# Kernel tuning notes

Measured on AMD Instinct MI355X. Metric: run time of the kernel, lower is better.

The kernel has to match this reference:

```python
import jax, jax.numpy as jnp
import numpy as np

N_NODES = 65536
N_GRAPHS = 1024
NODES_PER_G = 64
N_EDGES = 1048576
IN_FEATS = 512
HIDDEN = 1024
H4 = 256
EMB = 512
EPS = 1e-5
SLOPE = 0.01


def setup_inputs() -> dict:
    key = jax.random.key(0)
    ks = jax.random.split(key, 10)
    # within-graph random edges: edge e belongs to graph e // (E/B)
    epg = N_EDGES // N_GRAPHS
    eg = np.arange(N_EDGES) // epg
    rng = np.random.default_rng(0)
    src = rng.integers(0, NODES_PER_G, N_EDGES) + eg * NODES_PER_G
    dst = rng.integers(0, NODES_PER_G, N_EDGES) + eg * NODES_PER_G
    node_gid = np.arange(N_NODES) // NODES_PER_G
    return {
        "node_feats": jax.random.normal(ks[0], (N_NODES, IN_FEATS), jnp.float32),
        "edge_weights": jax.random.uniform(ks[1], (N_EDGES,), jnp.float32),
        "W1": jax.random.normal(ks[2], (IN_FEATS, HIDDEN), jnp.float32) * 0.05,
        "W2": jax.random.normal(ks[3], (HIDDEN, H4), jnp.float32) * 0.05,
        "W_emb": jax.random.normal(ks[4], (IN_FEATS + HIDDEN + H4, EMB), jnp.float32) * 0.02,
        "gn1_alpha": jnp.ones((HIDDEN,), jnp.float32),
        "gn1_gamma": jnp.ones((HIDDEN,), jnp.float32),
        "gn1_beta": jnp.zeros((HIDDEN,), jnp.float32),
        "gn2_alpha": jnp.ones((H4,), jnp.float32),
        "gn2_gamma": jnp.ones((H4,), jnp.float32),
        "gn2_beta": jnp.zeros((H4,), jnp.float32),
        "edge_src": jnp.asarray(src, jnp.int32),
        "edge_dst": jnp.asarray(dst, jnp.int32),
        "node_gid": jnp.asarray(node_gid, jnp.int32),
    }


def _seg_sum(x, ids, num):
    return jax.ops.segment_sum(x, ids, num_segments=num)


def _graph_conv(x, W, src, dst, ew):
    # DGL GraphConv, norm='both', bias=False, with edge_weight (u_mul_e)
    ones = jnp.ones((src.shape[0],), x.dtype)
    deg_out = jnp.clip(_seg_sum(ones, src, N_NODES), 1.0)
    deg_in = jnp.clip(_seg_sum(ones, dst, N_NODES), 1.0)
    h = (x * jax.lax.rsqrt(deg_out)[:, None]) @ W
    msg = h[src] * ew[:, None]
    agg = _seg_sum(msg, dst, N_NODES)
    return agg * jax.lax.rsqrt(deg_in)[:, None]


def _graph_norm(x, gid, counts, alpha, gamma, beta):
    # GraphNorm (Cai et al.): learnable mean-scale alpha, per-graph stats
    mean = _seg_sum(x, gid, N_GRAPHS) / counts[:, None]
    sub = x - alpha * mean[gid]
    var = _seg_sum(sub * sub, gid, N_GRAPHS) / counts[:, None]
    return gamma * sub * jax.lax.rsqrt(var[gid] + EPS) + beta


def _mean_nodes(x, gid, counts):
    return _seg_sum(x, gid, N_GRAPHS) / counts[:, None]


def _leaky(x):
    return jnp.where(x >= 0, x, SLOPE * x)


def reference(node_feats, edge_weights, W1, W2, W_emb,
              gn1_alpha, gn1_gamma, gn1_beta,
              gn2_alpha, gn2_gamma, gn2_beta,
              edge_src, edge_dst, node_gid):
    counts = jnp.clip(_seg_sum(jnp.ones((N_NODES,), node_feats.dtype), node_gid, N_GRAPHS), 1.0)
    r0 = _mean_nodes(node_feats, node_gid, counts)                 # [B, in]
    h1 = _graph_conv(node_feats, W1, edge_src, edge_dst, edge_weights)
    h1 = _leaky(_graph_norm(h1, node_gid, counts, gn1_alpha, gn1_gamma, gn1_beta))
    r1 = _mean_nodes(h1, node_gid, counts)                          # [B, hidden]
    h2 = _graph_conv(h1, W2, edge_src, edge_dst, edge_weights)
    h2 = _leaky(_graph_norm(h2, node_gid, counts, gn2_alpha, gn2_gamma, gn2_beta))
    r2 = _mean_nodes(h2, node_gid, counts)                          # [B, hidden/4]
    emb = jnp.concatenate([r0, r1, r2], axis=1) @ W_emb             # [B, EMB]
    # InstanceNorm1d on [B, E] input: per-row normalization, no affine
    mu = jnp.mean(emb, axis=1, keepdims=True)
    var = jnp.mean((emb - mu) ** 2, axis=1, keepdims=True)
    emb = (emb - mu) * jax.lax.rsqrt(var + EPS)
    return _leaky(emb)
```

## Files before the change

### kernel.cpp

```cpp
#include <hip/hip_runtime.h>
#include <hip/hip_bf16.h>
#include <stdint.h>

#define N_NODES   65536
#define N_GRAPHS  1024
#define N_EDGES   1048576
#define IN_FEATS  512
#define HIDDEN    1024
#define H4        256
#define EMB_DIM   512
#define RDIM      1792
#define EPS_F     1e-5f
#define SLOPE_F   0.01f

typedef __bf16 bf16;
typedef __bf16 bf16x8 __attribute__((ext_vector_type(8)));
typedef float  floatx4 __attribute__((ext_vector_type(4)));

#define GLDS16(gp, lp) __builtin_amdgcn_global_load_lds( \
    (const __attribute__((address_space(1))) void*)(gp), \
    (__attribute__((address_space(3))) void*)(lp), 16, 0, 0)

__global__ __launch_bounds__(256) void k_graph_build(
    const int* __restrict__ src, const int* __restrict__ dst,
    const float* __restrict__ ew,
    bf16* __restrict__ adjb, float* __restrict__ scl_o)
{
    __shared__ float sAdj[4096];
    __shared__ float sDegO[64], sDegI[64];
    int g = blockIdx.x, tid = threadIdx.x;
    for (int i = tid; i < 4096; i += 256) sAdj[i] = 0.f;
    if (tid < 64) { sDegO[tid] = 0.f; sDegI[tid] = 0.f; }
    __syncthreads();
    int e0 = g * 1024;
    #pragma unroll
    for (int i = 0; i < 4; ++i) {
        int e = e0 + i * 256 + tid;
        int s = src[e] & 63, d = dst[e] & 63;
        atomicAdd(&sAdj[(d << 6) | s], ew[e]);
        atomicAdd(&sDegO[s], 1.f);
        atomicAdd(&sDegI[d], 1.f);
    }
    __syncthreads();
    if (tid < 64) scl_o[g * 64 + tid] = rsqrtf(fmaxf(sDegO[tid], 1.f));
    bf16* ag = adjb + ((size_t)g << 12);
    for (int i = tid; i < 4096; i += 256) {
        float si = rsqrtf(fmaxf(sDegI[i >> 6], 1.f));
        ag[i] = (bf16)(sAdj[i] * si);
    }
}

__global__ __launch_bounds__(256) void k_transpose(
    const float* __restrict__ W, bf16* __restrict__ WT, int K, int logN)
{
    int idx = blockIdx.x * 256 + threadIdx.x;
    if (idx >= (K << logN)) return;
    int n = idx & ((1 << logN) - 1);
    int k = idx >> logN;
    WT[(size_t)n * K + k] = (bf16)W[idx];
}

__global__ __launch_bounds__(256) void k_prep_agg1(
    const float* __restrict__ x, const float* __restrict__ so,
    const bf16* __restrict__ adjb,
    bf16* __restrict__ axs1, bf16* __restrict__ Rb)
{
    __shared__ __align__(16) bf16 sOut[64 * 264];
    __shared__ float sSo[64];
    int g = blockIdx.x >> 1, half = blockIdx.x & 1;
    int tid = threadIdx.x, lane = tid & 63, wave = tid >> 6, q = lane >> 4;
    if (tid < 64) sSo[tid] = so[g * 64 + tid];
    const float* xg = x + (size_t)g * 64 * IN_FEATS + half * 256;
    const bf16* ag = adjb + ((size_t)g << 12);

    bf16x8 af[4][2];
    #pragma unroll
    for (int mt = 0; mt < 4; ++mt)
        #pragma unroll
        for (int kk = 0; kk < 2; ++kk)
            af[mt][kk] = *(const bf16x8*)&ag[(mt * 16 + (lane & 15)) * 64 + kk * 32 + q * 8];
    __syncthreads();
    float sov[2][8];
    #pragma unroll
    for (int kk = 0; kk < 2; ++kk)
        #pragma unroll
        for (int j = 0; j < 8; ++j) sov[kk][j] = sSo[kk * 32 + q * 8 + j];

    #pragma unroll
    for (int nt = 0; nt < 4; ++nt) {
        int cl = wave * 64 + nt * 16 + (lane & 15);
        floatx4 acc[4] = {};
        float r0 = 0.f;
        #pragma unroll
        for (int kk = 0; kk < 2; ++kk) {
            bf16x8 bfrag;
            #pragma unroll
            for (int j = 0; j < 8; ++j) {
                float v = xg[(size_t)(kk * 32 + q * 8 + j) * IN_FEATS + cl];
                r0 += v;
                bfrag[j] = (bf16)(v * sov[kk][j]);
            }
            #pragma unroll
            for (int mt = 0; mt < 4; ++mt)
                acc[mt] = __builtin_amdgcn_mfma_f32_16x16x32_bf16(af[mt][kk], bfrag, acc[mt], 0, 0, 0);
        }
        r0 += __shfl_xor(r0, 16);
        r0 += __shfl_xor(r0, 32);
        if (lane < 16) Rb[(size_t)g * RDIM + half * 256 + cl] = (bf16)(r0 * (1.f / 64.f));
        #pragma unroll
        for (int mt = 0; mt < 4; ++mt)
            #pragma unroll
            for (int i = 0; i < 4; ++i)
                sOut[(mt * 16 + q * 4 + i) * 264 + cl] = (bf16)acc[mt][i];
    }
    __syncthreads();
    #pragma unroll
    for (int it = 0; it < 8; ++it) {
        int idx = it * 256 + tid;
        int d = idx >> 5, c8 = idx & 31;
        *(bf16x8*)&axs1[(size_t)(g * 64 + d) * IN_FEATS + half * 256 + c8 * 8] =
            *(const bf16x8*)&sOut[d * 264 + c8 * 8];
    }
}

__device__ __forceinline__ void gemm_mainloop(
    const bf16* __restrict__ A, const bf16* __restrict__ BT, int K,
    int row0, int col0, int lane, int wave, int wm, int wn, int q,
    bf16* sA, bf16* sB, floatx4 (&acc)[4][4])
{
    for (int k0 = 0; k0 < K; k0 += 64) {
        #pragma unroll
        for (int i = 0; i < 4; ++i) {
            int u = (wave * 4 + i) * 64 + lane;
            int r = u >> 3, p = u & 7;
            int c = p ^ (r & 7);
            GLDS16(A  + (size_t)(row0 + r) * K + (k0 + c * 8), &sA[(wave * 4 + i) * 512]);
            GLDS16(BT + (size_t)(col0 + r) * K + (k0 + c * 8), &sB[(wave * 4 + i) * 512]);
        }
        asm volatile("s_waitcnt vmcnt(0)" ::: "memory");
        __syncthreads();
        #pragma unroll
        for (int kk = 0; kk < 64; kk += 32) {
            bf16x8 afr[4], bfr[4];
            #pragma unroll
            for (int mt = 0; mt < 4; ++mt) {
                int r = wm * 64 + mt * 16 + (lane & 15);
                int c = (kk >> 3) + q;
                afr[mt] = *(const bf16x8*)&sA[(r * 8 + (c ^ (r & 7))) * 8];
            }
            #pragma unroll
            for (int nt = 0; nt < 4; ++nt) {
                int r = wn * 64 + nt * 16 + (lane & 15);
                int c = (kk >> 3) + q;
                bfr[nt] = *(const bf16x8*)&sB[(r * 8 + (c ^ (r & 7))) * 8];
            }
            #pragma unroll
            for (int mt = 0; mt < 4; ++mt)
                #pragma unroll
                for (int nt = 0; nt < 4; ++nt)
                    acc[mt][nt] = __builtin_amdgcn_mfma_f32_16x16x32_bf16(
                        afr[mt], bfr[nt], acc[mt][nt], 0, 0, 0);
        }
        __syncthreads();
    }
}

__device__ __forceinline__ void swizzle_block(int cb, int& bx, int& by)
{
    int b = blockIdx.y * gridDim.x + blockIdx.x;
    int xcd = b & 7, t = b >> 3;
    bx = t % cb;
    by = (t / cb) * 8 + xcd;
}

__global__ __launch_bounds__(256) void k_gemm1_f(
    const bf16* __restrict__ A, const bf16* __restrict__ BT,
    const float* __restrict__ alpha, const float* __restrict__ gamma,
    const float* __restrict__ beta,
    const float* __restrict__ so,
    bf16* __restrict__ xs2, bf16* __restrict__ Rb)
{
    __shared__ __align__(16) bf16 sm[128 * 136];
    __shared__ float sSo[128];
    bf16* sA = sm;
    bf16* sB = sm + 8192;
    const int tid = threadIdx.x;
    const int lane = tid & 63, wave = tid >> 6, q = lane >> 4;
    const int wm = wave & 1, wn = wave >> 1;
    int bx, by; swizzle_block(gridDim.x, bx, by);
    const int row0 = by * 128, col0 = bx * 128;

    if (tid < 128) sSo[tid] = so[row0 + tid];

    floatx4 acc[4][4] = {};
    gemm_mainloop(A, BT, IN_FEATS, row0, col0, lane, wave, wm, wn, q, sA, sB, acc);

    const int gw = by * 2 + wm;
    bf16* sOut = sm;
    #pragma unroll
    for (int nt = 0; nt < 4; ++nt) {
        int cl = wn * 64 + nt * 16 + (lane & 15);
        int colg = col0 + cl;
        float lsum = 0.f;
        #pragma unroll
        for (int mt = 0; mt < 4; ++mt)
            #pragma unroll
            for (int i = 0; i < 4; ++i) lsum += acc[mt][nt][i];
        lsum += __shfl_xor(lsum, 16);
        lsum += __shfl_xor(lsum, 32);
        float am = alpha[colg] * (lsum * (1.f / 64.f));
        float gm = gamma[colg], bt = beta[colg];
        float sub[4][4], qv = 0.f;
        #pragma unroll
        for (int mt = 0; mt < 4; ++mt)
            #pragma unroll
            for (int i = 0; i < 4; ++i) {
                float d = acc[mt][nt][i] - am;
                sub[mt][i] = d; qv += d * d;
            }
        qv += __shfl_xor(qv, 16);
        qv += __shfl_xor(qv, 32);
        float rs = rsqrtf(qv * (1.f / 64.f) + EPS_F);
        float rsum = 0.f;
        #pragma unroll
        for (int mt = 0; mt < 4; ++mt)
            #pragma unroll
            for (int i = 0; i < 4; ++i) {
                float o = gm * sub[mt][i] * rs + bt;
                o = (o >= 0.f) ? o : SLOPE_F * o;
                rsum += o;
                int r = wm * 64 + mt * 16 + q * 4 + i;
                sOut[r * 136 + cl] = (bf16)(o * sSo[r]);
            }
        rsum += __shfl_xor(rsum, 16);
        rsum += __shfl_xor(rsum, 32);
        if (lane < 16)
            Rb[(size_t)gw * RDIM + 512 + colg] = (bf16)(rsum * (1.f / 64.f));
    }
    __syncthreads();
    #pragma unroll
    for (int it = 0; it < 8; ++it) {
        int idx = it * 256 + tid;
        int r = idx >> 4, c8 = idx & 15;
        *(bf16x8*)&xs2[(size_t)(row0 + r) * HIDDEN + col0 + c8 * 8] =
            *(const bf16x8*)&sOut[r * 136 + c8 * 8];
    }
}

__global__ __launch_bounds__(256) void k_gemm2_f(
    const bf16* __restrict__ A, const bf16* __restrict__ BT,
    const bf16* __restrict__ adjb,
    const float* __restrict__ alpha, const float* __restrict__ gamma,
    const float* __restrict__ beta,
    bf16* __restrict__ Rb)
{
    __shared__ __align__(16) bf16 sm[128 * 136];
    bf16* sA = sm;
    bf16* sB = sm + 8192;
    const int tid = threadIdx.x;
    const int lane = tid & 63, wave = tid >> 6, q = lane >> 4;
    const int wm = wave & 1, wn = wave >> 1;
    int bx, by; swizzle_block(gridDim.x, bx, by);
    const int row0 = by * 128, col0 = bx * 128;

    floatx4 acc[4][4] = {};
    gemm_mainloop(A, BT, HIDDEN, row0, col0, lane, wave, wm, wn, q, sA, sB, acc);

    bf16* sT = sm;
    #pragma unroll
    for (int nt = 0; nt < 4; ++nt) {
        int cl = wn * 64 + nt * 16 + (lane & 15);
        #pragma unroll
        for (int mt = 0; mt < 4; ++mt)
            #pragma unroll
            for (int i = 0; i < 4; ++i)
                sT[cl * 136 + wm * 64 + mt * 16 + q * 4 + i] = (bf16)acc[mt][nt][i];
    }
    asm volatile("s_waitcnt lgkmcnt(0)" ::: "memory");

    const int gw = by * 2 + wm;
    const bf16* ag = adjb + ((size_t)gw << 12);
    floatx4 a2[4][4] = {};
    #pragma unroll
    for (int kk = 0; kk < 2; ++kk) {
        bf16x8 afr[4], bfr[4];
        #pragma unroll
        for (int mt = 0; mt < 4; ++mt)
            afr[mt] = *(const bf16x8*)&ag[(mt * 16 + (lane & 15)) * 64 + kk * 32 + q * 8];
        #pragma unroll
        for (int nt = 0; nt < 4; ++nt)
            bfr[nt] = *(const bf16x8*)&sT[(wn * 64 + nt * 16 + (lane & 15)) * 136 + wm * 64 + kk * 32 + q * 8];
        #pragma unroll
        for (int mt = 0; mt < 4; ++mt)
            #pragma unroll
            for (int nt = 0; nt < 4; ++nt)
                a2[mt][nt] = __builtin_amdgcn_mfma_f32_16x16x32_bf16(afr[mt], bfr[nt], a2[mt][nt], 0, 0, 0);
    }

    #pragma unroll
    for (int nt = 0; nt < 4; ++nt) {
        int colg = col0 + wn * 64 + nt * 16 + (lane & 15);
        float lsum = 0.f;
        #pragma unroll
        for (int mt = 0; mt < 4; ++mt)
            #pragma unroll
            for (int i = 0; i < 4; ++i) lsum += a2[mt][nt][i];
        lsum += __shfl_xor(lsum, 16);
        lsum += __shfl_xor(lsum, 32);
        float am = alpha[colg] * (lsum * (1.f / 64.f));
        float gm = gamma[colg], bt = beta[colg];
        float sub[4][4], qv = 0.f;
        #pragma unroll
        for (int mt = 0; mt < 4; ++mt)
            #pragma unroll
            for (int i = 0; i < 4; ++i) {
                float d = a2[mt][nt][i] - am;
                sub[mt][i] = d; qv += d * d;
            }
        qv += __shfl_xor(qv, 16);
        qv += __shfl_xor(qv, 32);
        float rs = rsqrtf(qv * (1.f / 64.f) + EPS_F);
        float rsum = 0.f;
        #pragma unroll
        for (int mt = 0; mt < 4; ++mt)
            #pragma unroll
            for (int i = 0; i < 4; ++i) {
                float o = gm * sub[mt][i] * rs + bt;
                rsum += (o >= 0.f) ? o : SLOPE_F * o;
            }
        rsum += __shfl_xor(rsum, 16);
        rsum += __shfl_xor(rsum, 32);
        if (lane < 16)
            Rb[(size_t)gw * RDIM + 1536 + colg] = (bf16)(rsum * (1.f / 64.f));
    }
}

__global__ __launch_bounds__(256) void k_gemm_ro(
    const bf16* __restrict__ A, const bf16* __restrict__ BT,
    float* __restrict__ Cout)
{
    __shared__ __align__(16) bf16 sm[16384];
    bf16* sA = sm;
    bf16* sB = sm + 8192;
    const int tid = threadIdx.x;
    const int lane = tid & 63, wave = tid >> 6, q = lane >> 4;
    const int wm = wave & 1, wn = wave >> 1;
    int bx, by; swizzle_block(gridDim.x, bx, by);
    const int row0 = by * 128, col0 = bx * 128;

    floatx4 acc[4][4] = {};
    gemm_mainloop(A, BT, RDIM, row0, col0, lane, wave, wm, wn, q, sA, sB, acc);

    #pragma unroll
    for (int mt = 0; mt < 4; ++mt)
        #pragma unroll
        for (int nt = 0; nt < 4; ++nt) {
            int col = col0 + wn * 64 + nt * 16 + (lane & 15);
            #pragma unroll
            for (int i = 0; i < 4; ++i) {
                int row = row0 + wm * 64 + mt * 16 + q * 4 + i;
                Cout[(size_t)row * EMB_DIM + col] = acc[mt][nt][i];
            }
        }
}

__global__ __launch_bounds__(256) void k_instnorm(
    const float* __restrict__ emb, float* __restrict__ out)
{
    int row = blockIdx.x, tid = threadIdx.x;
    int lane = tid & 63, wave = tid >> 6;
    __shared__ float sS[4], sQ[4];
    float v0 = emb[(size_t)row * EMB_DIM + tid];
    float v1 = emb[(size_t)row * EMB_DIM + 256 + tid];
    float s = v0 + v1, q = v0 * v0 + v1 * v1;
    #pragma unroll
    for (int off = 32; off; off >>= 1) {
        s += __shfl_down(s, off);
        q += __shfl_down(q, off);
    }
    if (lane == 0) { sS[wave] = s; sQ[wave] = q; }
    __syncthreads();
    float S = sS[0] + sS[1] + sS[2] + sS[3];
    float Q = sQ[0] + sQ[1] + sQ[2] + sQ[3];
    float mu = S * (1.f / 512.f);
    float var = Q * (1.f / 512.f) - mu * mu;
    float rs = rsqrtf(var + EPS_F);
    float o0 = (v0 - mu) * rs; o0 = (o0 >= 0.f) ? o0 : SLOPE_F * o0;
    float o1 = (v1 - mu) * rs; o1 = (o1 >= 0.f) ? o1 : SLOPE_F * o1;
    out[(size_t)row * EMB_DIM + tid]       = o0;
    out[(size_t)row * EMB_DIM + 256 + tid] = o1;
}

extern "C" void kernel_launch(void* const* d_in, const int* in_sizes, int n_in,
                              void* d_out, int out_size, void* d_ws, size_t ws_size,
                              hipStream_t stream) {
    const float* x    = (const float*)d_in[0];
    const float* ew   = (const float*)d_in[1];
    const float* W1   = (const float*)d_in[2];
    const float* W2   = (const float*)d_in[3];
    const float* Wemb = (const float*)d_in[4];
    const float* a1   = (const float*)d_in[5];
    const float* g1   = (const float*)d_in[6];
    const float* b1   = (const float*)d_in[7];
    const float* a2   = (const float*)d_in[8];
    const float* g2   = (const float*)d_in[9];
    const float* b2   = (const float*)d_in[10];
    const int* esrc   = (const int*)d_in[11];
    const int* edst   = (const int*)d_in[12];
    float* out = (float*)d_out;

    char* ws = (char*)d_ws;
    const size_t MB = 1024ull * 1024ull;
    bf16*  adjb   = (bf16*)(ws);
    float* scl_o  = (float*)(ws + 8 * MB);
    bf16*  Rb     = (bf16*)(ws + 9 * MB);
    bf16*  W1T    = (bf16*)(ws + 13 * MB);
    bf16*  W2T    = (bf16*)(ws + 14 * MB);
    bf16*  WembT  = (bf16*)(ws + 15 * MB);
    float* emb    = (float*)(ws + 17 * MB);
    bf16*  axs1   = (bf16*)(ws + 20 * MB);
    bf16*  xs2    = (bf16*)(ws + 84 * MB);

    k_graph_build<<<N_GRAPHS, 256, 0, stream>>>(esrc, edst, ew, adjb, scl_o);
    k_transpose<<<2048, 256, 0, stream>>>(W1, W1T, 512, 10);
    k_transpose<<<1024, 256, 0, stream>>>(W2, W2T, 1024, 8);
    k_transpose<<<3584, 256, 0, stream>>>(Wemb, WembT, 1792, 9);

    k_prep_agg1<<<N_GRAPHS * 2, 256, 0, stream>>>(x, scl_o, adjb, axs1, Rb);

    k_gemm1_f<<<dim3(HIDDEN / 128, N_NODES / 128), 256, 0, stream>>>(
        axs1, W1T, a1, g1, b1, scl_o, xs2, Rb);
    k_gemm2_f<<<dim3(H4 / 128, N_NODES / 128), 256, 0, stream>>>(
        xs2, W2T, adjb, a2, g2, b2, Rb);
    k_gemm_ro<<<dim3(EMB_DIM / 128, N_GRAPHS / 128), 256, 0, stream>>>(
        Rb, WembT, emb);
    k_instnorm<<<N_GRAPHS, 256, 0, stream>>>(emb, out);

    (void)in_sizes; (void)n_in; (void)out_size; (void)ws_size;
}
```

Measured before the change: 490.7 us.

## Fuse layer-1 and layer-2 GEMMs into a per-graph kernel keeping hidden activations on-chip

Replaces the separate GEMM1 (with GraphNorm epilogue writing xs2 to global memory) and GEMM2 kernels with a single per-graph kernel. Each block loads its graph's 64x512 aggregated inputs into LDS, computes hidden features in 128-column chunks, applies GraphNorm, LeakyReLU and readout, then immediately accumulates the chunk into the layer-2 product. The layer-2 aggregation and norm run in the same block. This removes the 128MB xs2 round trip and one launch. In exchange, B fragments of W1T and W2T are read directly from global or L2 without LDS staging, and each block is serialised over 8 chunks with only 1024 blocks, which may lower occupancy and MFMA efficiency.

```diff
diff --git a/kernel.cpp b/kernel.cpp
--- a/kernel.cpp
+++ b/kernel.cpp
@@ -21,6 +21,8 @@
     (const __attribute__((address_space(1))) void*)(gp), \
     (__attribute__((address_space(3))) void*)(lp), 16, 0, 0)
 
+#define MFMA16(a, b, c) __builtin_amdgcn_mfma_f32_16x16x32_bf16((a), (b), (c), 0, 0, 0)
+
 __global__ __launch_bounds__(256) void k_graph_build(
     const int* __restrict__ src, const int* __restrict__ dst,
     const float* __restrict__ ew,
@@ -102,7 +104,7 @@
             }
             #pragma unroll
             for (int mt = 0; mt < 4; ++mt)
-                acc[mt] = __builtin_amdgcn_mfma_f32_16x16x32_bf16(af[mt][kk], bfrag, acc[mt], 0, 0, 0);
+                acc[mt] = MFMA16(af[mt][kk], bfrag, acc[mt]);
         }
         r0 += __shfl_xor(r0, 16);
         r0 += __shfl_xor(r0, 32);
@@ -120,6 +122,197 @@
         int d = idx >> 5, c8 = idx & 31;
         *(bf16x8*)&axs1[(size_t)(g * 64 + d) * IN_FEATS + half * 256 + c8 * 8] =
             *(const bf16x8*)&sOut[d * 264 + c8 * 8];
+    }
+}
+
+__global__ __launch_bounds__(256) void k_fused12(
+    const bf16* __restrict__ axs1, const bf16* __restrict__ W1T,
+    const bf16* __restrict__ W2T,  const bf16* __restrict__ adjb,
+    const float* __restrict__ so,
+    const float* __restrict__ a1v, const float* __restrict__ g1v,
+    const float* __restrict__ b1v,
+    const float* __restrict__ a2v, const float* __restrict__ g2v,
+    const float* __restrict__ b2v,
+    bf16* __restrict__ Rb)
+{
+    __shared__ __align__(16) bf16 sm[40960];
+    bf16* sA = sm;
+    bf16* sX = sm + 32768;
+
+    const int g = blockIdx.x, tid = threadIdx.x;
+    const int lane = tid & 63, wave = tid >> 6, q = lane >> 4, l15 = lane & 15;
+
+    const bf16* Ag = axs1 + (((size_t)g << 6) * IN_FEATS);
+    #pragma unroll
+    for (int i = 0; i < 16; ++i) {
+        int u = i * 256 + tid;
+        int r = u >> 6, cp = u & 63;
+        int c = cp ^ (r & 63);
+        GLDS16(Ag + ((size_t)r << 9) + (c << 3), &sA[(i * 256 + wave * 64) * 8]);
+    }
+    float sov[16];
+    #pragma unroll
+    for (int mt = 0; mt < 4; ++mt)
+        #pragma unroll
+        for (int i = 0; i < 4; ++i)
+            sov[mt * 4 + i] = so[g * 64 + mt * 16 + q * 4 + i];
+
+    floatx4 h2[4][4] = {};
+
+    asm volatile("s_waitcnt vmcnt(0)" ::: "memory");
+    __syncthreads();
+
+    for (int c = 0; c < 8; ++c) {
+        floatx4 acc[4][2] = {};
+        #pragma unroll 4
+        for (int ks = 0; ks < 16; ++ks) {
+            bf16x8 bfr[2];
+            #pragma unroll
+            for (int nt = 0; nt < 2; ++nt) {
+                int n = c * 128 + wave * 32 + nt * 16 + l15;
+                bfr[nt] = *(const bf16x8*)&W1T[((size_t)n << 9) + ks * 32 + q * 8];
+            }
+            bf16x8 afr[4];
+            #pragma unroll
+            for (int mt = 0; mt < 4; ++mt) {
+                int r = mt * 16 + l15;
+                int cu = (ks * 4 + q) ^ (r & 63);
+                afr[mt] = *(const bf16x8*)&sA[(r * 64 + cu) * 8];
+            }
+            #pragma unroll
+            for (int mt = 0; mt < 4; ++mt)
+                #pragma unroll
+                for (int nt = 0; nt < 2; ++nt)
+                    acc[mt][nt] = MFMA16(afr[mt], bfr[nt], acc[mt][nt]);
+        }
+        #pragma unroll
+        for (int nt = 0; nt < 2; ++nt) {
+            int cl = wave * 32 + nt * 16 + l15;
+            int colg = c * 128 + cl;
+            float lsum = 0.f;
+            #pragma unroll
+            for (int mt = 0; mt < 4; ++mt)
+                #pragma unroll
+                for (int i = 0; i < 4; ++i) lsum += acc[mt][nt][i];
+            lsum += __shfl_xor(lsum, 16);
+            lsum += __shfl_xor(lsum, 32);
+            float am = a1v[colg] * (lsum * (1.f / 64.f));
+            float gm = g1v[colg], bt = b1v[colg];
+            float sub[4][4], qv = 0.f;
+            #pragma unroll
+            for (int mt = 0; mt < 4; ++mt)
+                #pragma unroll
+                for (int i = 0; i < 4; ++i) {
+                    float d = acc[mt][nt][i] - am;
+                    sub[mt][i] = d; qv += d * d;
+                }
+            qv += __shfl_xor(qv, 16);
+            qv += __shfl_xor(qv, 32);
+            float rs = rsqrtf(qv * (1.f / 64.f) + EPS_F);
+            float rsum = 0.f;
+            int cu = cl >> 3, ce = cl & 7;
+            #pragma unroll
+            for (int mt = 0; mt < 4; ++mt)
+                #pragma unroll
+                for (int i = 0; i < 4; ++i) {
+                    float o = gm * sub[mt][i] * rs + bt;
+                    o = (o >= 0.f) ? o : SLOPE_F * o;
+                    rsum += o;
+                    int r = mt * 16 + q * 4 + i;
+                    sX[(r * 16 + (cu ^ (r & 15))) * 8 + ce] = (bf16)(o * sov[mt * 4 + i]);
+                }
+            rsum += __shfl_xor(rsum, 16);
+            rsum += __shfl_xor(rsum, 32);
+            if (lane < 16)
+                Rb[(size_t)g * RDIM + 512 + colg] = (bf16)(rsum * (1.f / 64.f));
+        }
+        __syncthreads();
+        #pragma unroll
+        for (int kk = 0; kk < 4; ++kk) {
+            bf16x8 afr[4], bfr[4];
+            #pragma unroll
+            for (int mt = 0; mt < 4; ++mt) {
+                int r = mt * 16 + l15;
+                int cu = (kk * 4 + q) ^ (r & 15);
+                afr[mt] = *(const bf16x8*)&sX[(r * 16 + cu) * 8];
+            }
+            #pragma unroll
+            for (int nt = 0; nt < 4; ++nt) {
+                int n = wave * 64 + nt * 16 + l15;
+                bfr[nt] = *(const bf16x8*)&W2T[((size_t)n << 10) + c * 128 + kk * 32 + q * 8];
+            }
+            #pragma unroll
+            for (int mt = 0; mt < 4; ++mt)
+                #pragma unroll
+                for (int nt = 0; nt < 4; ++nt)
+                    h2[mt][nt] = MFMA16(afr[mt], bfr[nt], h2[mt][nt]);
+        }
+        __syncthreads();
+    }
+
+    bf16* sT = sA + wave * (64 * 68);
+    #pragma unroll
+    for (int nt = 0; nt < 4; ++nt) {
+        int cl = nt * 16 + l15;
+        #pragma unroll
+        for (int mt = 0; mt < 4; ++mt)
+            #pragma unroll
+            for (int i = 0; i < 4; ++i)
+                sT[cl * 68 + mt * 16 + q * 4 + i] = (bf16)h2[mt][nt][i];
+    }
+    asm volatile("s_waitcnt lgkmcnt(0)" ::: "memory");
+    const bf16* ag = adjb + ((size_t)g << 12);
+    floatx4 fin[4][4] = {};
+    #pragma unroll
+    for (int kk = 0; kk < 2; ++kk) {
+        bf16x8 afr[4], bfr[4];
+        #pragma unroll
+        for (int mt = 0; mt < 4; ++mt)
+            afr[mt] = *(const bf16x8*)&ag[(mt * 16 + l15) * 64 + kk * 32 + q * 8];
+        #pragma unroll
+        for (int nt = 0; nt < 4; ++nt)
+            bfr[nt] = *(const bf16x8*)&sT[(nt * 16 + l15) * 68 + kk * 32 + q * 8];
+        #pragma unroll
+        for (int mt = 0; mt < 4; ++mt)
+            #pragma unroll
+            for (int nt = 0; nt < 4; ++nt)
+                fin[mt][nt] = MFMA16(afr[mt], bfr[nt], fin[mt][nt]);
+    }
+    #pragma unroll
+    for (int nt = 0; nt < 4; ++nt) {
+        int colg = wave * 64 + nt * 16 + l15;
+        float lsum = 0.f;
+        #pragma unroll
+        for (int mt = 0; mt < 4; ++mt)
+            #pragma unroll
+            for (int i = 0; i < 4; ++i) lsum += fin[mt][nt][i];
+        lsum += __shfl_xor(lsum, 16);
+        lsum += __shfl_xor(lsum, 32);
+        float am = a2v[colg] * (lsum * (1.f / 64.f));
+        float gm = g2v[colg], bt = b2v[colg];
+        float sub[4][4], qv = 0.f;
+        #pragma unroll
+        for (int mt = 0; mt < 4; ++mt)
+            #pragma unroll
+            for (int i = 0; i < 4; ++i) {
+                float d = fin[mt][nt][i] - am;
+                sub[mt][i] = d; qv += d * d;
+            }
+        qv += __shfl_xor(qv, 16);
+        qv += __shfl_xor(qv, 32);
+        float rs = rsqrtf(qv * (1.f / 64.f) + EPS_F);
+        float rsum = 0.f;
+        #pragma unroll
+        for (int mt = 0; mt < 4; ++mt)
+            #pragma unroll
+            for (int i = 0; i < 4; ++i) {
+                float o = gm * sub[mt][i] * rs + bt;
+                rsum += (o >= 0.f) ? o : SLOPE_F * o;
+            }
+        rsum += __shfl_xor(rsum, 16);
+        rsum += __shfl_xor(rsum, 32);
+        if (lane < 16)
+            Rb[(size_t)g * RDIM + 1536 + colg] = (bf16)(rsum * (1.f / 64.f));
     }
 }
 
@@ -158,180 +351,9 @@
             for (int mt = 0; mt < 4; ++mt)
                 #pragma unroll
                 for (int nt = 0; nt < 4; ++nt)
-                    acc[mt][nt] = __builtin_amdgcn_mfma_f32_16x16x32_bf16(
-                        afr[mt], bfr[nt], acc[mt][nt], 0, 0, 0);
+                    acc[mt][nt] = MFMA16(afr[mt], bfr[nt], acc[mt][nt]);
         }
         __syncthreads();
-    }
-}
-
-__device__ __forceinline__ void swizzle_block(int cb, int& bx, int& by)
-{
-    int b = blockIdx.y * gridDim.x + blockIdx.x;
-    int xcd = b & 7, t = b >> 3;
-    bx = t % cb;
-    by = (t / cb) * 8 + xcd;
-}
-
-__global__ __launch_bounds__(256) void k_gemm1_f(
-    const bf16* __restrict__ A, const bf16* __restrict__ BT,
-    const float* __restrict__ alpha, const float* __restrict__ gamma,
-    const float* __restrict__ beta,
-    const float* __restrict__ so,
-    bf16* __restrict__ xs2, bf16* __restrict__ Rb)
-{
-    __shared__ __align__(16) bf16 sm[128 * 136];
-    __shared__ float sSo[128];
-    bf16* sA = sm;
-    bf16* sB = sm + 8192;
-    const int tid = threadIdx.x;
-    const int lane = tid & 63, wave = tid >> 6, q = lane >> 4;
-    const int wm = wave & 1, wn = wave >> 1;
-    int bx, by; swizzle_block(gridDim.x, bx, by);
-    const int row0 = by * 128, col0 = bx * 128;
-
-    if (tid < 128) sSo[tid] = so[row0 + tid];
-
-    floatx4 acc[4][4] = {};
-    gemm_mainloop(A, BT, IN_FEATS, row0, col0, lane, wave, wm, wn, q, sA, sB, acc);
-
-    const int gw = by * 2 + wm;
-    bf16* sOut = sm;
-    #pragma unroll
-    for (int nt = 0; nt < 4; ++nt) {
-        int cl = wn * 64 + nt * 16 + (lane & 15);
-        int colg = col0 + cl;
-        float lsum = 0.f;
-        #pragma unroll
-        for (int mt = 0; mt < 4; ++mt)
-            #pragma unroll
-            for (int i = 0; i < 4; ++i) lsum += acc[mt][nt][i];
-        lsum += __shfl_xor(lsum, 16);
-        lsum += __shfl_xor(lsum, 32);
-        float am = alpha[colg] * (lsum * (1.f / 64.f));
-        float gm = gamma[colg], bt = beta[colg];
-        float sub[4][4], qv = 0.f;
-        #pragma unroll
-        for (int mt = 0; mt < 4; ++mt)
-            #pragma unroll
-            for (int i = 0; i < 4; ++i) {
-                float d = acc[mt][nt][i] - am;
-                sub[mt][i] = d; qv += d * d;
-            }
-        qv += __shfl_xor(qv, 16);
-        qv += __shfl_xor(qv, 32);
-        float rs = rsqrtf(qv * (1.f / 64.f) + EPS_F);
-        float rsum = 0.f;
-        #pragma unroll
-        for (int mt = 0; mt < 4; ++mt)
-            #pragma unroll
-            for (int i = 0; i < 4; ++i) {
-                float o = gm * sub[mt][i] * rs + bt;
-                o = (o >= 0.f) ? o : SLOPE_F * o;
-                rsum += o;
-                int r = wm * 64 + mt * 16 + q * 4 + i;
-                sOut[r * 136 + cl] = (bf16)(o * sSo[r]);
-            }
-        rsum += __shfl_xor(rsum, 16);
-        rsum += __shfl_xor(rsum, 32);
-        if (lane < 16)
-            Rb[(size_t)gw * RDIM + 512 + colg] = (bf16)(rsum * (1.f / 64.f));
-    }
-    __syncthreads();
-    #pragma unroll
-    for (int it = 0; it < 8; ++it) {
-        int idx = it * 256 + tid;
-        int r = idx >> 4, c8 = idx & 15;
-        *(bf16x8*)&xs2[(size_t)(row0 + r) * HIDDEN + col0 + c8 * 8] =
-            *(const bf16x8*)&sOut[r * 136 + c8 * 8];
-    }
-}
-
-__global__ __launch_bounds__(256) void k_gemm2_f(
-    const bf16* __restrict__ A, const bf16* __restrict__ BT,
-    const bf16* __restrict__ adjb,
-    const float* __restrict__ alpha, const float* __restrict__ gamma,
-    const float* __restrict__ beta,
-    bf16* __restrict__ Rb)
-{
-    __shared__ __align__(16) bf16 sm[128 * 136];
-    bf16* sA = sm;
-    bf16* sB = sm + 8192;
-    const int tid = threadIdx.x;
-    const int lane = tid & 63, wave = tid >> 6, q = lane >> 4;
-    const int wm = wave & 1, wn = wave >> 1;
-    int bx, by; swizzle_block(gridDim.x, bx, by);
-    const int row0 = by * 128, col0 = bx * 128;
-
-    floatx4 acc[4][4] = {};
-    gemm_mainloop(A, BT, HIDDEN, row0, col0, lane, wave, wm, wn, q, sA, sB, acc);
-
-    bf16* sT = sm;
-    #pragma unroll
-    for (int nt = 0; nt < 4; ++nt) {
-        int cl = wn * 64 + nt * 16 + (lane & 15);
-        #pragma unroll
-        for (int mt = 0; mt < 4; ++mt)
-            #pragma unroll
-            for (int i = 0; i < 4; ++i)
-                sT[cl * 136 + wm * 64 + mt * 16 + q * 4 + i] = (bf16)acc[mt][nt][i];
-    }
-    asm volatile("s_waitcnt lgkmcnt(0)" ::: "memory");
-
-    const int gw = by * 2 + wm;
-    const bf16* ag = adjb + ((size_t)gw << 12);
-    floatx4 a2[4][4] = {};
-    #pragma unroll
-    for (int kk = 0; kk < 2; ++kk) {
-        bf16x8 afr[4], bfr[4];
-        #pragma unroll
-        for (int mt = 0; mt < 4; ++mt)
-            afr[mt] = *(const bf16x8*)&ag[(mt * 16 + (lane & 15)) * 64 + kk * 32 + q * 8];
-        #pragma unroll
-        for (int nt = 0; nt < 4; ++nt)
-            bfr[nt] = *(const bf16x8*)&sT[(wn * 64 + nt * 16 + (lane & 15)) * 136 + wm * 64 + kk * 32 + q * 8];
-        #pragma unroll
-        for (int mt = 0; mt < 4; ++mt)
-            #pragma unroll
-            for (int nt = 0; nt < 4; ++nt)
-                a2[mt][nt] = __builtin_amdgcn_mfma_f32_16x16x32_bf16(afr[mt], bfr[nt], a2[mt][nt], 0, 0, 0);
-    }
-
-    #pragma unroll
-    for (int nt = 0; nt < 4; ++nt) {
-        int colg = col0 + wn * 64 + nt * 16 + (lane & 15);
-        float lsum = 0.f;
-        #pragma unroll
-        for (int mt = 0; mt < 4; ++mt)
-            #pragma unroll
-            for (int i = 0; i < 4; ++i) lsum += a2[mt][nt][i];
-        lsum += __shfl_xor(lsum, 16);
-        lsum += __shfl_xor(lsum, 32);
-        float am = alpha[colg] * (lsum * (1.f / 64.f));
-        float gm = gamma[colg], bt = beta[colg];
-        float sub[4][4], qv = 0.f;
-        #pragma unroll
-        for (int mt = 0; mt < 4; ++mt)
-            #pragma unroll
-            for (int i = 0; i < 4; ++i) {
-                float d = a2[mt][nt][i] - am;
-                sub[mt][i] = d; qv += d * d;
-            }
-        qv += __shfl_xor(qv, 16);
-        qv += __shfl_xor(qv, 32);
-        float rs = rsqrtf(qv * (1.f / 64.f) + EPS_F);
-        float rsum = 0.f;
-        #pragma unroll
-        for (int mt = 0; mt < 4; ++mt)
-            #pragma unroll
-            for (int i = 0; i < 4; ++i) {
-                float o = gm * sub[mt][i] * rs + bt;
-                rsum += (o >= 0.f) ? o : SLOPE_F * o;
-            }
-        rsum += __shfl_xor(rsum, 16);
-        rsum += __shfl_xor(rsum, 32);
-        if (lane < 16)
-            Rb[(size_t)gw * RDIM + 1536 + colg] = (bf16)(rsum * (1.f / 64.f));
     }
 }
 
@@ -345,8 +367,7 @@
     const int tid = threadIdx.x;
     const int lane = tid & 63, wave = tid >> 6, q = lane >> 4;
     const int wm = wave & 1, wn = wave >> 1;
-    int bx, by; swizzle_block(gridDim.x, bx, by);
-    const int row0 = by * 128, col0 = bx * 128;
+    const int row0 = blockIdx.y * 128, col0 = blockIdx.x * 128;
 
     floatx4 acc[4][4] = {};
     gemm_mainloop(A, BT, RDIM, row0, col0, lane, wave, wm, wn, q, sA, sB, acc);
@@ -419,7 +440,6 @@
     bf16*  WembT  = (bf16*)(ws + 15 * MB);
     float* emb    = (float*)(ws + 17 * MB);
     bf16*  axs1   = (bf16*)(ws + 20 * MB);
-    bf16*  xs2    = (bf16*)(ws + 84 * MB);
 
     k_graph_build<<<N_GRAPHS, 256, 0, stream>>>(esrc, edst, ew, adjb, scl_o);
     k_transpose<<<2048, 256, 0, stream>>>(W1, W1T, 512, 10);
@@ -428,10 +448,9 @@
 
     k_prep_agg1<<<N_GRAPHS * 2, 256, 0, stream>>>(x, scl_o, adjb, axs1, Rb);
 
-    k_gemm1_f<<<dim3(HIDDEN / 128, N_NODES / 128), 256, 0, stream>>>(
-        axs1, W1T, a1, g1, b1, scl_o, xs2, Rb);
-    k_gemm2_f<<<dim3(H4 / 128, N_NODES / 128), 256, 0, stream>>>(
-        xs2, W2T, adjb, a2, g2, b2, Rb);
+    k_fused12<<<N_GRAPHS, 256, 0, stream>>>(
+        axs1, W1T, W2T, adjb, scl_o, a1, g1, b1, a2, g2, b2, Rb);
+
     k_gemm_ro<<<dim3(EMB_DIM / 128, N_GRAPHS / 128), 256, 0, stream>>>(
         Rb, WembT, emb);
     k_instnorm<<<N_GRAPHS, 256, 0, stream>>>(emb, out);
```

Result: slower. 606.5 us (+23.6%).

## Retile gemm2 to one block per graph and merge weight transposes

Applied to the files above, without the earlier changes.

The second-layer GEMM now uses one block per graph, a 64x256 tile, so each block computes all H4 columns for its 64 nodes. The A rows are therefore read once rather than once per 128-column tile, and the per-wave aggregation and norm epilogue maps directly onto a graph. The three weight-transpose launches are merged into one kernel, and the block swizzle is dropped from the readout GEMM. The risks are fewer blocks (1024) with a larger B tile loaded per k-step into shared memory, and no double buffering.

```diff
diff --git a/kernel.cpp b/kernel.cpp
--- a/kernel.cpp
+++ b/kernel.cpp
@@ -21,6 +21,8 @@
     (const __attribute__((address_space(1))) void*)(gp), \
     (__attribute__((address_space(3))) void*)(lp), 16, 0, 0)
 
+#define MFMA16(a, b, c) __builtin_amdgcn_mfma_f32_16x16x32_bf16((a), (b), (c), 0, 0, 0)
+
 __global__ __launch_bounds__(256) void k_graph_build(
     const int* __restrict__ src, const int* __restrict__ dst,
     const float* __restrict__ ew,
@@ -50,14 +52,24 @@
     }
 }
 
-__global__ __launch_bounds__(256) void k_transpose(
-    const float* __restrict__ W, bf16* __restrict__ WT, int K, int logN)
+__global__ __launch_bounds__(256) void k_transpose_all(
+    const float* __restrict__ W1, const float* __restrict__ W2,
+    const float* __restrict__ Wemb,
+    bf16* __restrict__ W1T, bf16* __restrict__ W2T, bf16* __restrict__ WembT)
 {
     int idx = blockIdx.x * 256 + threadIdx.x;
-    if (idx >= (K << logN)) return;
-    int n = idx & ((1 << logN) - 1);
-    int k = idx >> logN;
-    WT[(size_t)n * K + k] = (bf16)W[idx];
+    if (idx < 524288) {
+        int n = idx & 1023, k = idx >> 10;
+        W1T[(size_t)n * 512 + k] = (bf16)W1[idx];
+    } else if (idx < 786432) {
+        int i = idx - 524288;
+        int n = i & 255, k = i >> 8;
+        W2T[(size_t)n * 1024 + k] = (bf16)W2[i];
+    } else {
+        int i = idx - 786432;
+        int n = i & 511, k = i >> 9;
+        WembT[(size_t)n * 1792 + k] = (bf16)Wemb[i];
+    }
 }
 
 __global__ __launch_bounds__(256) void k_prep_agg1(
@@ -102,7 +114,7 @@
             }
             #pragma unroll
             for (int mt = 0; mt < 4; ++mt)
-                acc[mt] = __builtin_amdgcn_mfma_f32_16x16x32_bf16(af[mt][kk], bfrag, acc[mt], 0, 0, 0);
+                acc[mt] = MFMA16(af[mt][kk], bfrag, acc[mt]);
         }
         r0 += __shfl_xor(r0, 16);
         r0 += __shfl_xor(r0, 32);
@@ -158,8 +170,7 @@
             for (int mt = 0; mt < 4; ++mt)
                 #pragma unroll
                 for (int nt = 0; nt < 4; ++nt)
-                    acc[mt][nt] = __builtin_amdgcn_mfma_f32_16x16x32_bf16(
-                        afr[mt], bfr[nt], acc[mt][nt], 0, 0, 0);
+                    acc[mt][nt] = MFMA16(afr[mt], bfr[nt], acc[mt][nt]);
         }
         __syncthreads();
     }
@@ -254,52 +265,89 @@
     const float* __restrict__ beta,
     bf16* __restrict__ Rb)
 {
-    __shared__ __align__(16) bf16 sm[128 * 136];
+    __shared__ __align__(16) bf16 sm[20480];
     bf16* sA = sm;
-    bf16* sB = sm + 8192;
-    const int tid = threadIdx.x;
-    const int lane = tid & 63, wave = tid >> 6, q = lane >> 4;
-    const int wm = wave & 1, wn = wave >> 1;
-    int bx, by; swizzle_block(gridDim.x, bx, by);
-    const int row0 = by * 128, col0 = bx * 128;
+    bf16* sB = sm + 4096;
+    const int g = blockIdx.x, tid = threadIdx.x;
+    const int lane = tid & 63, wave = tid >> 6, q = lane >> 4, l15 = lane & 15;
 
     floatx4 acc[4][4] = {};
-    gemm_mainloop(A, BT, HIDDEN, row0, col0, lane, wave, wm, wn, q, sA, sB, acc);
-
-    bf16* sT = sm;
+    const bf16* Ag = A + ((size_t)g << 6) * HIDDEN;
+
+    for (int k0 = 0; k0 < HIDDEN; k0 += 64) {
+        {
+            #pragma unroll
+            for (int i = 0; i < 2; ++i) {
+                int u = i * 256 + tid;
+                int r = u >> 3, c = (u & 7) ^ (r & 7);
+                GLDS16(Ag + (size_t)r * HIDDEN + (k0 + c * 8), &sA[(i * 256 + wave * 64) * 8]);
+            }
+            #pragma unroll
+            for (int i = 0; i < 8; ++i) {
+                int u = i * 256 + tid;
+                int r = u >> 3, c = (u & 7) ^ (r & 7);
+                GLDS16(BT + (size_t)r * HIDDEN + (k0 + c * 8), &sB[(i * 256 + wave * 64) * 8]);
+            }
+        }
+        asm volatile("s_waitcnt vmcnt(0)" ::: "memory");
+        __syncthreads();
+        #pragma unroll
+        for (int kk = 0; kk < 64; kk += 32) {
+            bf16x8 afr[4], bfr[4];
+            #pragma unroll
+            for (int mt = 0; mt < 4; ++mt) {
+                int r = mt * 16 + l15;
+                int c = (kk >> 3) + q;
+                afr[mt] = *(const bf16x8*)&sA[(r * 8 + (c ^ (r & 7))) * 8];
+            }
+            #pragma unroll
+            for (int nt = 0; nt < 4; ++nt) {
+                int r = wave * 64 + nt * 16 + l15;
+                int c = (kk >> 3) + q;
+                bfr[nt] = *(const bf16x8*)&sB[(r * 8 + (c ^ (r & 7))) * 8];
+            }
+            #pragma unroll
+            for (int mt = 0; mt < 4; ++mt)
+                #pragma unroll
+                for (int nt = 0; nt < 4; ++nt)
+                    acc[mt][nt] = MFMA16(afr[mt], bfr[nt], acc[mt][nt]);
+        }
+        __syncthreads();
+    }
+
+    bf16* sT = sm + wave * (64 * 68);
     #pragma unroll
     for (int nt = 0; nt < 4; ++nt) {
-        int cl = wn * 64 + nt * 16 + (lane & 15);
+        int cl = nt * 16 + l15;
         #pragma unroll
         for (int mt = 0; mt < 4; ++mt)
             #pragma unroll
             for (int i = 0; i < 4; ++i)
-                sT[cl * 136 + wm * 64 + mt * 16 + q * 4 + i] = (bf16)acc[mt][nt][i];
+                sT[cl * 68 + mt * 16 + q * 4 + i] = (bf16)acc[mt][nt][i];
     }
     asm volatile("s_waitcnt lgkmcnt(0)" ::: "memory");
 
-    const int gw = by * 2 + wm;
-    const bf16* ag = adjb + ((size_t)gw << 12);
+    const bf16* ag = adjb + ((size_t)g << 12);
     floatx4 a2[4][4] = {};
     #pragma unroll
     for (int kk = 0; kk < 2; ++kk) {
         bf16x8 afr[4], bfr[4];
         #pragma unroll
         for (int mt = 0; mt < 4; ++mt)
-            afr[mt] = *(const bf16x8*)&ag[(mt * 16 + (lane & 15)) * 64 + kk * 32 + q * 8];
+            afr[mt] = *(const bf16x8*)&ag[(mt * 16 + l15) * 64 + kk * 32 + q * 8];
         #pragma unroll
         for (int nt = 0; nt < 4; ++nt)
-            bfr[nt] = *(const bf16x8*)&sT[(wn * 64 + nt * 16 + (lane & 15)) * 136 + wm * 64 + kk * 32 + q * 8];
+            bfr[nt] = *(const bf16x8*)&sT[(nt * 16 + l15) * 68 + kk * 32 + q * 8];
         #pragma unroll
         for (int mt = 0; mt < 4; ++mt)
             #pragma unroll
             for (int nt = 0; nt < 4; ++nt)
-                a2[mt][nt] = __builtin_amdgcn_mfma_f32_16x16x32_bf16(afr[mt], bfr[nt], a2[mt][nt], 0, 0, 0);
+                a2[mt][nt] = MFMA16(afr[mt], bfr[nt], a2[mt][nt]);
     }
 
     #pragma unroll
     for (int nt = 0; nt < 4; ++nt) {
-        int colg = col0 + wn * 64 + nt * 16 + (lane & 15);
+        int colg = wave * 64 + nt * 16 + l15;
         float lsum = 0.f;
         #pragma unroll
         for (int mt = 0; mt < 4; ++mt)
@@ -331,7 +379,7 @@
         rsum += __shfl_xor(rsum, 16);
         rsum += __shfl_xor(rsum, 32);
         if (lane < 16)
-            Rb[(size_t)gw * RDIM + 1536 + colg] = (bf16)(rsum * (1.f / 64.f));
+            Rb[(size_t)g * RDIM + 1536 + colg] = (bf16)(rsum * (1.f / 64.f));
     }
 }
 
@@ -345,8 +393,7 @@
     const int tid = threadIdx.x;
     const int lane = tid & 63, wave = tid >> 6, q = lane >> 4;
     const int wm = wave & 1, wn = wave >> 1;
-    int bx, by; swizzle_block(gridDim.x, bx, by);
-    const int row0 = by * 128, col0 = bx * 128;
+    const int row0 = blockIdx.y * 128, col0 = blockIdx.x * 128;
 
     floatx4 acc[4][4] = {};
     gemm_mainloop(A, BT, RDIM, row0, col0, lane, wave, wm, wn, q, sA, sB, acc);
@@ -422,15 +469,13 @@
     bf16*  xs2    = (bf16*)(ws + 84 * MB);
 
     k_graph_build<<<N_GRAPHS, 256, 0, stream>>>(esrc, edst, ew, adjb, scl_o);
-    k_transpose<<<2048, 256, 0, stream>>>(W1, W1T, 512, 10);
-    k_transpose<<<1024, 256, 0, stream>>>(W2, W2T, 1024, 8);
-    k_transpose<<<3584, 256, 0, stream>>>(Wemb, WembT, 1792, 9);
+    k_transpose_all<<<6656, 256, 0, stream>>>(W1, W2, Wemb, W1T, W2T, WembT);
 
     k_prep_agg1<<<N_GRAPHS * 2, 256, 0, stream>>>(x, scl_o, adjb, axs1, Rb);
 
     k_gemm1_f<<<dim3(HIDDEN / 128, N_NODES / 128), 256, 0, stream>>>(
         axs1, W1T, a1, g1, b1, scl_o, xs2, Rb);
-    k_gemm2_f<<<dim3(H4 / 128, N_NODES / 128), 256, 0, stream>>>(
+    k_gemm2_f<<<N_GRAPHS, 256, 0, stream>>>(
         xs2, W2T, adjb, a2, g2, b2, Rb);
     k_gemm_ro<<<dim3(EMB_DIM / 128, N_GRAPHS / 128), 256, 0, stream>>>(
         Rb, WembT, emb);
```

Result: no change. 491.7 us (+0.2%).
